# Optimization experiments

Measured on AMD Instinct MI355X. Metric: run time of the kernel, lower is better.

Reference implementation:

```python
import jax, jax.numpy as jnp
import numpy as np

MAX_TIMESTEPS = 100
EPS_VAR = 1e-8
EPS_DEN = 1e-8

def setup_inputs() -> dict:
    key = jax.random.key(0)
    k1, k2, k3, k4, k5 = jax.random.split(key, 5)
    b, c, h, w = 64, 3, 256, 256
    data = jax.random.normal(k1, (b, c, h, w), dtype=jnp.float32)
    noise = jax.random.normal(k2, (b, c, h, w), dtype=jnp.float32)
    times = jax.random.uniform(k3, (b,), dtype=jnp.float32)
    pred_mean = jax.random.normal(k4, (b, c, h, w), dtype=jnp.float32)
    pred_log_var = jax.random.normal(k5, (b, c, h, w), dtype=jnp.float32)
    return {"data": data, "noise": noise, "times": times,
            "pred_mean": pred_mean, "pred_log_var": pred_log_var}

def reference(data, noise, times, pred_mean, pred_log_var):
    b = data.shape[0]
    # times scaled as in forward: t * (1 - max_timesteps^-1)
    t = times * (1.0 - MAX_TIMESTEPS ** (-1))          # [b]
    t4 = t[:, None, None, None]                         # [b,1,1,1]
    tb = t[:, None]                                     # [b,1]

    # noised = noise.lerp(data, t) = noise + t*(data - noise)
    noised = noise + t4 * (data - noise)                # [b,c,h,w]

    d_flat = data.reshape(b, -1)                        # [j, d]
    n_flat = noised.reshape(b, -1)                      # [b, d]

    # dist[b,j] = sum_chw (noised_b - t_b * data_j)^2 / (2 * var_b)
    # expanded to avoid materializing [b,j,c,h,w]:
    var = (1.0 - tb) ** 2 + EPS_VAR                     # [b,1]
    n2 = jnp.sum(n_flat * n_flat, axis=-1, keepdims=True)   # [b,1]
    d2 = jnp.sum(d_flat * d_flat, axis=-1)                   # [j]
    cross = n_flat @ d_flat.T                                # [b,j]
    dist = (n2 - 2.0 * tb * cross + (tb ** 2) * d2[None, :]) / (2.0 * var)

    weights = jax.nn.softmax(-dist, axis=1)             # [b,j]

    # u_hat = sum_j w_bj (data_j - noised_b) / (1 - t_b + eps)
    #       = (weights @ data - noised) / (1 - t_b + eps)   (weights row-sum to 1)
    mix = weights @ d_flat                              # [b,d]
    u_hat = ((mix - n_flat) / (1.0 - tb + EPS_DEN)).reshape(data.shape)

    flow_cond = data - noise
    correction = jax.lax.stop_gradient(u_hat ** 2 - flow_cond ** 2)

    pred_var = jnp.exp(pred_log_var)
    loss = ((pred_mean - flow_cond) ** 2 / (2.0 * pred_var)
            + 0.5 * pred_log_var
            + correction / (2.0 * pred_var))
    loss = jax.lax.stop_gradient(pred_var) * loss
    return loss.mean()
```

## Files before the change

### kernel.cpp

```cpp
#include <hip/hip_runtime.h>
#include <cstdint>

namespace {

constexpr int BB = 64;
constexpr int DDIM = 196608;
constexpr float T_SCALE = 0.99f;

constexpr int WS_ZD   = 0;
constexpr int WS_DD   = 4096;
constexpr int WS_Z2   = 8192;
constexpr int WS_ELEM = 8256;
constexpr int NRED    = 8257;
constexpr int WS_U2   = 8320;
constexpr int WS_BIGP = 8384;
constexpr int PSTRIDE = 8272;

using f32x4  = __attribute__((ext_vector_type(4))) float;
using bf16x8 = __attribute__((ext_vector_type(8))) __bf16;

__device__ inline f32x4 MFMA(bf16x8 a, bf16x8 b, f32x4 c) {
  return __builtin_amdgcn_mfma_f32_16x16x32_bf16(a, b, c, 0, 0, 0);
}

__global__ void k_init(float* __restrict__ ws) {
  int idx = blockIdx.x * 256 + threadIdx.x;
  if (idx < NRED) ws[idx] = 0.0f;
}

template <int SUBT, bool ATOMIC>
__global__ __launch_bounds__(512) void k_main(
    const float* __restrict__ data, const float* __restrict__ noise,
    const float* __restrict__ pmean, const float* __restrict__ plogv,
    float* __restrict__ ws, float* __restrict__ bigp) {
  __shared__ __align__(16) short lds[6 * 4096];
  __shared__ float esm[8];

  const int t  = threadIdx.x;
  const int wv = t >> 6;
  const int l  = t & 63;
  const int g  = wv >> 2;
  const int m0 = (wv & 3) << 4;
  const int sr = t >> 3;
  const int c0 = t & 7;
  const int chunk0 = blockIdx.x * (SUBT << 6);
  float* dst = ATOMIC ? ws : (bigp + (size_t)blockIdx.x * PSTRIDE);

  f32x4 acc[4];
#pragma unroll
  for (int b = 0; b < 4; ++b) acc[b] = 0.0f;
  float z2acc = 0.0f, eacc = 0.0f;
  float4 dv[2], zv[2], pv[2], gv[2];
  uint4 sZ[3], sD[3];

  auto LOAD = [&](int s) {
    const size_t base = (size_t)sr * DDIM + chunk0 + (s << 6) + (c0 << 3);
#pragma unroll
    for (int i = 0; i < 2; ++i) {
      dv[i] = *(const float4*)(data  + base + (i << 2));
      zv[i] = *(const float4*)(noise + base + (i << 2));
      pv[i] = *(const float4*)(pmean + base + (i << 2));
      gv[i] = *(const float4*)(plogv + base + (i << 2));
    }
  };

  auto SPLIT8 = [&](const float4* v, uint4& H, uint4& M, uint4& L) {
    uint32_t h[4], m[4], lo[4];
    const float* f = (const float*)v;
#pragma unroll
    for (int p = 0; p < 4; ++p) {
      const float a = f[2 * p], b = f[2 * p + 1];
      const uint32_t ha = __float_as_uint(a) & 0xFFFF0000u;
      const uint32_t hb = __float_as_uint(b) & 0xFFFF0000u;
      h[p] = (ha >> 16) | hb;
      const float ra = a - __uint_as_float(ha);
      const float rb = b - __uint_as_float(hb);
      const uint32_t ma = __float_as_uint(ra) & 0xFFFF0000u;
      const uint32_t mb = __float_as_uint(rb) & 0xFFFF0000u;
      m[p] = (ma >> 16) | mb;
      const float sa = ra - __uint_as_float(ma);
      const float sb = rb - __uint_as_float(mb);
      lo[p] = (__float_as_uint(sa) >> 16) | (__float_as_uint(sb) & 0xFFFF0000u);
    }
    H = uint4{h[0], h[1], h[2], h[3]};
    M = uint4{m[0], m[1], m[2], m[3]};
    L = uint4{lo[0], lo[1], lo[2], lo[3]};
  };

  auto SPLITCALC = [&]() {
    const float* df = (const float*)dv;
    const float* zf = (const float*)zv;
    const float* pf = (const float*)pv;
    const float* gf = (const float*)gv;
#pragma unroll
    for (int p = 0; p < 8; ++p) {
      const float d = df[p], z = zf[p], pm = pf[p], pl = gf[p];
      const float fc = d - z;
      eacc += 0.5f * (pm * pm + __expf(pl) * pl) - pm * fc;
      z2acc += z * z;
    }
    SPLIT8(zv, sZ[0], sZ[1], sZ[2]);
    SPLIT8(dv, sD[0], sD[1], sD[2]);
  };

  auto DSW = [&]() {
    char* base = (char*)lds + sr * 128 + ((c0 ^ (sr & 7)) << 4);
#pragma unroll
    for (int sp = 0; sp < 3; ++sp) {
      *(uint4*)(base + sp * 8192)       = sZ[sp];
      *(uint4*)(base + (3 + sp) * 8192) = sD[sp];
    }
  };

  auto MMA = [&]() {
#pragma unroll
    for (int s2 = 0; s2 < 2; ++s2) {
      const int rA   = m0 + (l & 15);
      const int cA   = (s2 << 2) + (l >> 4);
      const int offA = rA * 128 + ((cA ^ (rA & 7)) << 4);
      bf16x8 af[3];
#pragma unroll
      for (int sp = 0; sp < 3; ++sp)
        af[sp] = *(const bf16x8*)((const char*)lds + (g * 3 + sp) * 8192 + offA);
#pragma unroll
      for (int b = 0; b < 4; ++b) {
        const int rB   = (b << 4) + (l & 15);
        const int offB = rB * 128 + ((cA ^ (rB & 7)) << 4);
        bf16x8 bd[3];
#pragma unroll
        for (int sp = 0; sp < 3; ++sp)
          bd[sp] = *(const bf16x8*)((const char*)lds + (3 + sp) * 8192 + offB);
        acc[b] = MFMA(af[0], bd[0], acc[b]);
        acc[b] = MFMA(af[0], bd[1], acc[b]);
        acc[b] = MFMA(af[1], bd[0], acc[b]);
        acc[b] = MFMA(af[1], bd[1], acc[b]);
        acc[b] = MFMA(af[0], bd[2], acc[b]);
        acc[b] = MFMA(af[2], bd[0], acc[b]);
      }
    }
  };

  LOAD(0);
  SPLITCALC();
  DSW();
  LOAD(1);
  __syncthreads();

  for (int s = 0; s < SUBT; ++s) {
    if (s + 1 < SUBT) SPLITCALC();
    MMA();
    __syncthreads();
    if (s + 1 < SUBT) {
      DSW();
      if (s + 2 < SUBT) LOAD(s + 2);
      __syncthreads();
    }
  }

  {
    float v = z2acc;
    v += __shfl_xor(v, 1);
    v += __shfl_xor(v, 2);
    v += __shfl_xor(v, 4);
    if ((l & 7) == 0) {
      if (ATOMIC) atomicAdd(ws + WS_Z2 + sr, v);
      else        dst[WS_Z2 + sr] = v;
    }
  }
  {
    float ev = eacc;
#pragma unroll
    for (int m = 1; m <= 32; m <<= 1) ev += __shfl_xor(ev, m);
    if (l == 0) esm[wv] = ev;
  }
  __syncthreads();
  if (t == 0) {
    float s0 = 0.f;
#pragma unroll
    for (int e = 0; e < 8; ++e) s0 += esm[e];
    if (ATOMIC) atomicAdd(ws + WS_ELEM, s0);
    else        dst[WS_ELEM] = s0;
  }

  const int grOff = (g == 0) ? WS_ZD : WS_DD;
#pragma unroll
  for (int b = 0; b < 4; ++b)
#pragma unroll
    for (int rg = 0; rg < 4; ++rg) {
      const int row = m0 + ((l >> 4) << 2) + rg;
      const int col = (b << 4) + (l & 15);
      if (ATOMIC) atomicAdd(ws + grOff + row * 64 + col, acc[b][rg]);
      else        dst[grOff + row * 64 + col] = acc[b][rg];
    }
}

__global__ void k_reduce(const float* __restrict__ bigp, float* __restrict__ ws,
                         int nb) {
  const int idx = blockIdx.x * 64 + threadIdx.x;
  if (idx >= NRED) return;
  const int per = nb >> 3;
  const size_t b0 = (size_t)blockIdx.y * per;
  float s = 0.f;
#pragma unroll 4
  for (int b = 0; b < per; ++b)
    s += bigp[(b0 + b) * PSTRIDE + idx];
  atomicAdd(ws + idx, s);
}

__global__ void k_small(const float* __restrict__ times, float* __restrict__ ws) {
  const int i = blockIdx.x;
  const int j = threadIdx.x;
  const double tt = (double)(times[i] * T_SCALE);
  const double omt = 1.0 - tt;
  const double var = omt * omt + 1e-8;
  const double inv2v = 1.0 / (2.0 * var);
  const double zd = (double)ws[WS_ZD + (i << 6) + j];
  const double dd = (double)ws[WS_DD + (i << 6) + j];
  const double cross = omt * zd + tt * dd;
  const double d2j = (double)ws[WS_DD + j * 65];
  const double lg = (2.0 * tt * cross - tt * tt * d2j) * inv2v;
  double m = lg;
#pragma unroll
  for (int msk = 1; msk <= 32; msk <<= 1) m = fmax(m, __shfl_xor(m, msk));
  const double e = exp(lg - m);
  double S = e;
#pragma unroll
  for (int msk = 1; msk <= 32; msk <<= 1) S += __shfl_xor(S, msk);
  const double wgt = e / S;

  __shared__ double wsh[64];
  wsh[j] = wgt;
  __syncthreads();
  double inner = 0.0;
#pragma unroll 8
  for (int j2 = 0; j2 < 64; ++j2)
    inner += wsh[j2] * (double)ws[WS_DD + (j << 6) + j2];
  double s1 = wgt * inner;
  double s2 = wgt * cross;
#pragma unroll
  for (int msk = 1; msk <= 32; msk <<= 1) {
    s1 += __shfl_xor(s1, msk);
    s2 += __shfl_xor(s2, msk);
  }
  if (j == 0) {
    const double zdii = (double)ws[WS_ZD + i * 65];
    const double d2i  = (double)ws[WS_DD + i * 65];
    const double z2i  = (double)ws[WS_Z2 + i];
    const double n2   = omt * omt * z2i + 2.0 * tt * omt * zdii + tt * tt * d2i;
    const double den  = omt + 1e-8;
    ws[WS_U2 + i] = (float)((s1 - 2.0 * s2 + n2) / (den * den));
  }
}

__global__ void k_final(const float* __restrict__ ws, float* __restrict__ out) {
  const int t = threadIdx.x;
  double v = 0.5 * (double)ws[WS_U2 + t];
  if (t == 0) v += (double)ws[WS_ELEM];
#pragma unroll
  for (int m = 1; m <= 32; m <<= 1) v += __shfl_xor(v, m);
  if (t == 0) out[0] = (float)(v / (double)((size_t)BB * DDIM));
}

}

extern "C" void kernel_launch(void* const* d_in, const int* in_sizes, int n_in,
                              void* d_out, int out_size, void* d_ws, size_t ws_size,
                              hipStream_t stream) {
  const float* data  = (const float*)d_in[0];
  const float* noise = (const float*)d_in[1];
  const float* times = (const float*)d_in[2];
  const float* pmean = (const float*)d_in[3];
  const float* plogv = (const float*)d_in[4];
  float* out = (float*)d_out;
  float* ws  = (float*)d_ws;
  float* bigp = ws + WS_BIGP;

  const bool fits512 =
      ws_size >= ((size_t)WS_BIGP + (size_t)512 * PSTRIDE) * sizeof(float);

  k_init<<<dim3(33), dim3(256), 0, stream>>>(ws);
  if (fits512) {
    k_main<6, false><<<dim3(512), dim3(512), 0, stream>>>(
        data, noise, pmean, plogv, ws, bigp);
    k_reduce<<<dim3(130, 8), dim3(64), 0, stream>>>(bigp, ws, 512);
  } else {
    k_main<6, true><<<dim3(512), dim3(512), 0, stream>>>(
        data, noise, pmean, plogv, ws, bigp);
  }
  k_small<<<dim3(64), dim3(64), 0, stream>>>(times, ws);
  k_final<<<dim3(1), dim3(64), 0, stream>>>(ws, out);
}
```

Baseline: 58.84 us.

## Double-buffer LDS with smaller K-steps and fuse softmax and final kernels

The main kernel now stages 32-column K-slices into two alternating LDS buffers, so each step needs one barrier instead of two. Global loads of the next slice overlap the MFMA work on the current one, and SUBT doubles so the per-block coverage stays the same. The small softmax kernel and the final reduction are merged into one 1024-thread launch that uses shuffles instead of shared memory for the weights, which removes one kernel launch. In exchange each thread does narrower 8-byte LDS writes, the MFMA batches per step are smaller, and the fused tail runs as a single block.

```diff
diff --git a/kernel.cpp b/kernel.cpp
--- a/kernel.cpp
+++ b/kernel.cpp
@@ -12,7 +12,6 @@
 constexpr int WS_Z2   = 8192;
 constexpr int WS_ELEM = 8256;
 constexpr int NRED    = 8257;
-constexpr int WS_U2   = 8320;
 constexpr int WS_BIGP = 8384;
 constexpr int PSTRIDE = 8272;
 
@@ -33,7 +32,7 @@
     const float* __restrict__ data, const float* __restrict__ noise,
     const float* __restrict__ pmean, const float* __restrict__ plogv,
     float* __restrict__ ws, float* __restrict__ bigp) {
-  __shared__ __align__(16) short lds[6 * 4096];
+  __shared__ __align__(16) char lds[49152];
   __shared__ float esm[8];
 
   const int t  = threadIdx.x;
@@ -41,34 +40,28 @@
   const int l  = t & 63;
   const int g  = wv >> 2;
   const int m0 = (wv & 3) << 4;
-  const int sr = t >> 3;
-  const int c0 = t & 7;
-  const int chunk0 = blockIdx.x * (SUBT << 6);
+  const int r  = t >> 3;
+  const int c4 = t & 7;
+  const int chunk0 = blockIdx.x * (SUBT * 32);
   float* dst = ATOMIC ? ws : (bigp + (size_t)blockIdx.x * PSTRIDE);
 
   f32x4 acc[4];
 #pragma unroll
   for (int b = 0; b < 4; ++b) acc[b] = 0.0f;
   float z2acc = 0.0f, eacc = 0.0f;
-  float4 dv[2], zv[2], pv[2], gv[2];
-  uint4 sZ[3], sD[3];
-
-  auto LOAD = [&](int s) {
-    const size_t base = (size_t)sr * DDIM + chunk0 + (s << 6) + (c0 << 3);
-#pragma unroll
-    for (int i = 0; i < 2; ++i) {
-      dv[i] = *(const float4*)(data  + base + (i << 2));
-      zv[i] = *(const float4*)(noise + base + (i << 2));
-      pv[i] = *(const float4*)(pmean + base + (i << 2));
-      gv[i] = *(const float4*)(plogv + base + (i << 2));
-    }
-  };
-
-  auto SPLIT8 = [&](const float4* v, uint4& H, uint4& M, uint4& L) {
-    uint32_t h[4], m[4], lo[4];
-    const float* f = (const float*)v;
-#pragma unroll
-    for (int p = 0; p < 4; ++p) {
+  float4 dv, zv;
+
+  auto LOADDZ = [&](int s) {
+    const size_t off = (size_t)r * DDIM + chunk0 + (s << 5) + (c4 << 2);
+    dv = *(const float4*)(data  + off);
+    zv = *(const float4*)(noise + off);
+  };
+
+  auto SPLITW = [&](int buf, const float4& v, int tbase) {
+    const float* f = (const float*)&v;
+    uint32_t h[2], m[2], lo[2];
+#pragma unroll
+    for (int p = 0; p < 2; ++p) {
       const float a = f[2 * p], b = f[2 * p + 1];
       const uint32_t ha = __float_as_uint(a) & 0xFFFF0000u;
       const uint32_t hb = __float_as_uint(b) & 0xFFFF0000u;
@@ -82,79 +75,75 @@
       const float sb = rb - __uint_as_float(mb);
       lo[p] = (__float_as_uint(sa) >> 16) | (__float_as_uint(sb) & 0xFFFF0000u);
     }
-    H = uint4{h[0], h[1], h[2], h[3]};
-    M = uint4{m[0], m[1], m[2], m[3]};
-    L = uint4{lo[0], lo[1], lo[2], lo[3]};
-  };
-
-  auto SPLITCALC = [&]() {
-    const float* df = (const float*)dv;
-    const float* zf = (const float*)zv;
-    const float* pf = (const float*)pv;
-    const float* gf = (const float*)gv;
-#pragma unroll
-    for (int p = 0; p < 8; ++p) {
+#pragma unroll
+    for (int sp = 0; sp < 3; ++sp) {
+      const int tile = tbase + sp;
+      const int byte = buf + ((tile >> 1) << 13) + (r << 7) +
+                       (((((tile & 1) << 2) + (c4 >> 1)) ^ (r & 7)) << 4) +
+                       ((c4 & 1) << 3);
+      const uint32_t* pk = (sp == 0) ? h : (sp == 1) ? m : lo;
+      *(uint2*)(lds + byte) = uint2{pk[0], pk[1]};
+    }
+  };
+
+  auto STAGE = [&](int s) {
+    const int buf = (s & 1) * 24576;
+    const size_t off = (size_t)r * DDIM + chunk0 + (s << 5) + (c4 << 2);
+    const float4 pm4 = *(const float4*)(pmean + off);
+    const float4 pl4 = *(const float4*)(plogv + off);
+    SPLITW(buf, zv, 0);
+    SPLITW(buf, dv, 3);
+    const float* df = (const float*)&dv;
+    const float* zf = (const float*)&zv;
+    const float* pf = (const float*)&pm4;
+    const float* gf = (const float*)&pl4;
+#pragma unroll
+    for (int p = 0; p < 4; ++p) {
       const float d = df[p], z = zf[p], pm = pf[p], pl = gf[p];
-      const float fc = d - z;
-      eacc += 0.5f * (pm * pm + __expf(pl) * pl) - pm * fc;
+      eacc += 0.5f * (pm * pm + __expf(pl) * pl) - pm * (d - z);
       z2acc += z * z;
     }
-    SPLIT8(zv, sZ[0], sZ[1], sZ[2]);
-    SPLIT8(dv, sD[0], sD[1], sD[2]);
-  };
-
-  auto DSW = [&]() {
-    char* base = (char*)lds + sr * 128 + ((c0 ^ (sr & 7)) << 4);
-#pragma unroll
-    for (int sp = 0; sp < 3; ++sp) {
-      *(uint4*)(base + sp * 8192)       = sZ[sp];
-      *(uint4*)(base + (3 + sp) * 8192) = sD[sp];
-    }
-  };
-
-  auto MMA = [&]() {
-#pragma unroll
-    for (int s2 = 0; s2 < 2; ++s2) {
-      const int rA   = m0 + (l & 15);
-      const int cA   = (s2 << 2) + (l >> 4);
-      const int offA = rA * 128 + ((cA ^ (rA & 7)) << 4);
-      bf16x8 af[3];
-#pragma unroll
-      for (int sp = 0; sp < 3; ++sp)
-        af[sp] = *(const bf16x8*)((const char*)lds + (g * 3 + sp) * 8192 + offA);
-#pragma unroll
-      for (int b = 0; b < 4; ++b) {
-        const int rB   = (b << 4) + (l & 15);
-        const int offB = rB * 128 + ((cA ^ (rB & 7)) << 4);
-        bf16x8 bd[3];
-#pragma unroll
-        for (int sp = 0; sp < 3; ++sp)
-          bd[sp] = *(const bf16x8*)((const char*)lds + (3 + sp) * 8192 + offB);
-        acc[b] = MFMA(af[0], bd[0], acc[b]);
-        acc[b] = MFMA(af[0], bd[1], acc[b]);
-        acc[b] = MFMA(af[1], bd[0], acc[b]);
-        acc[b] = MFMA(af[1], bd[1], acc[b]);
-        acc[b] = MFMA(af[0], bd[2], acc[b]);
-        acc[b] = MFMA(af[2], bd[0], acc[b]);
-      }
-    }
-  };
-
-  LOAD(0);
-  SPLITCALC();
-  DSW();
-  LOAD(1);
+  };
+
+  auto FRAG = [&](int buf, int tile, int row) -> bf16x8 {
+    const int byte = buf + ((tile >> 1) << 13) + (row << 7) +
+                     (((((tile & 1) << 2) + (l >> 4)) ^ (row & 7)) << 4);
+    return *(const bf16x8*)(lds + byte);
+  };
+
+  auto MMA = [&](int s) {
+    const int buf = (s & 1) * 24576;
+    const int ar  = m0 + (l & 15);
+    bf16x8 af[3];
+#pragma unroll
+    for (int sp = 0; sp < 3; ++sp) af[sp] = FRAG(buf, g * 3 + sp, ar);
+#pragma unroll
+    for (int b = 0; b < 4; ++b) {
+      const int br = (b << 4) + (l & 15);
+      bf16x8 bd[3];
+#pragma unroll
+      for (int sp = 0; sp < 3; ++sp) bd[sp] = FRAG(buf, 3 + sp, br);
+      acc[b] = MFMA(af[0], bd[0], acc[b]);
+      acc[b] = MFMA(af[0], bd[1], acc[b]);
+      acc[b] = MFMA(af[1], bd[0], acc[b]);
+      acc[b] = MFMA(af[1], bd[1], acc[b]);
+      acc[b] = MFMA(af[0], bd[2], acc[b]);
+      acc[b] = MFMA(af[2], bd[0], acc[b]);
+    }
+  };
+
+  LOADDZ(0);
+  STAGE(0);
+  LOADDZ(1);
   __syncthreads();
 
   for (int s = 0; s < SUBT; ++s) {
-    if (s + 1 < SUBT) SPLITCALC();
-    MMA();
+    if (s + 1 < SUBT) {
+      STAGE(s + 1);
+      if (s + 2 < SUBT) LOADDZ(s + 2);
+    }
+    MMA(s);
     __syncthreads();
-    if (s + 1 < SUBT) {
-      DSW();
-      if (s + 2 < SUBT) LOAD(s + 2);
-      __syncthreads();
-    }
   }
 
   {
@@ -163,8 +152,8 @@
     v += __shfl_xor(v, 2);
     v += __shfl_xor(v, 4);
     if ((l & 7) == 0) {
-      if (ATOMIC) atomicAdd(ws + WS_Z2 + sr, v);
-      else        dst[WS_Z2 + sr] = v;
+      if (ATOMIC) atomicAdd(ws + WS_Z2 + r, v);
+      else        dst[WS_Z2 + r] = v;
     }
   }
   {
@@ -207,58 +196,63 @@
   atomicAdd(ws + idx, s);
 }
 
-__global__ void k_small(const float* __restrict__ times, float* __restrict__ ws) {
-  const int i = blockIdx.x;
-  const int j = threadIdx.x;
-  const double tt = (double)(times[i] * T_SCALE);
-  const double omt = 1.0 - tt;
-  const double var = omt * omt + 1e-8;
-  const double inv2v = 1.0 / (2.0 * var);
-  const double zd = (double)ws[WS_ZD + (i << 6) + j];
-  const double dd = (double)ws[WS_DD + (i << 6) + j];
-  const double cross = omt * zd + tt * dd;
-  const double d2j = (double)ws[WS_DD + j * 65];
-  const double lg = (2.0 * tt * cross - tt * tt * d2j) * inv2v;
-  double m = lg;
-#pragma unroll
-  for (int msk = 1; msk <= 32; msk <<= 1) m = fmax(m, __shfl_xor(m, msk));
-  const double e = exp(lg - m);
-  double S = e;
-#pragma unroll
-  for (int msk = 1; msk <= 32; msk <<= 1) S += __shfl_xor(S, msk);
-  const double wgt = e / S;
-
-  __shared__ double wsh[64];
-  wsh[j] = wgt;
+__global__ __launch_bounds__(1024) void k_smallfinal(
+    const float* __restrict__ times, const float* __restrict__ ws,
+    float* __restrict__ out) {
+  __shared__ double u2s[64];
+  const int t = threadIdx.x;
+  const int wv = t >> 6;
+  const int j = t & 63;
+
+#pragma unroll
+  for (int ii = 0; ii < 4; ++ii) {
+    const int i = (wv << 2) + ii;
+    const double tt = (double)(times[i] * T_SCALE);
+    const double omt = 1.0 - tt;
+    const double var = omt * omt + 1e-8;
+    const double inv2v = 1.0 / (2.0 * var);
+    const double zd = (double)ws[WS_ZD + (i << 6) + j];
+    const double dd = (double)ws[WS_DD + (i << 6) + j];
+    const double cross = omt * zd + tt * dd;
+    const double d2j = (double)ws[WS_DD + j * 65];
+    const double lg = (2.0 * tt * cross - tt * tt * d2j) * inv2v;
+    double m = lg;
+#pragma unroll
+    for (int msk = 1; msk <= 32; msk <<= 1) m = fmax(m, __shfl_xor(m, msk));
+    const double e = exp(lg - m);
+    double S = e;
+#pragma unroll
+    for (int msk = 1; msk <= 32; msk <<= 1) S += __shfl_xor(S, msk);
+    const double wgt = e / S;
+
+    double inner = 0.0;
+#pragma unroll 8
+    for (int j2 = 0; j2 < 64; ++j2)
+      inner += __shfl(wgt, j2) * (double)ws[WS_DD + (j << 6) + j2];
+    double s1 = wgt * inner;
+    double s2 = wgt * cross;
+#pragma unroll
+    for (int msk = 1; msk <= 32; msk <<= 1) {
+      s1 += __shfl_xor(s1, msk);
+      s2 += __shfl_xor(s2, msk);
+    }
+    if (j == 0) {
+      const double zdii = (double)ws[WS_ZD + i * 65];
+      const double d2i  = (double)ws[WS_DD + i * 65];
+      const double z2i  = (double)ws[WS_Z2 + i];
+      const double n2 = omt * omt * z2i + 2.0 * tt * omt * zdii + tt * tt * d2i;
+      const double den = omt + 1e-8;
+      u2s[i] = (s1 - 2.0 * s2 + n2) / (den * den);
+    }
+  }
   __syncthreads();
-  double inner = 0.0;
-#pragma unroll 8
-  for (int j2 = 0; j2 < 64; ++j2)
-    inner += wsh[j2] * (double)ws[WS_DD + (j << 6) + j2];
-  double s1 = wgt * inner;
-  double s2 = wgt * cross;
-#pragma unroll
-  for (int msk = 1; msk <= 32; msk <<= 1) {
-    s1 += __shfl_xor(s1, msk);
-    s2 += __shfl_xor(s2, msk);
-  }
-  if (j == 0) {
-    const double zdii = (double)ws[WS_ZD + i * 65];
-    const double d2i  = (double)ws[WS_DD + i * 65];
-    const double z2i  = (double)ws[WS_Z2 + i];
-    const double n2   = omt * omt * z2i + 2.0 * tt * omt * zdii + tt * tt * d2i;
-    const double den  = omt + 1e-8;
-    ws[WS_U2 + i] = (float)((s1 - 2.0 * s2 + n2) / (den * den));
-  }
-}
-
-__global__ void k_final(const float* __restrict__ ws, float* __restrict__ out) {
-  const int t = threadIdx.x;
-  double v = 0.5 * (double)ws[WS_U2 + t];
-  if (t == 0) v += (double)ws[WS_ELEM];
-#pragma unroll
-  for (int m = 1; m <= 32; m <<= 1) v += __shfl_xor(v, m);
-  if (t == 0) out[0] = (float)(v / (double)((size_t)BB * DDIM));
+  if (wv == 0) {
+    double v = 0.5 * u2s[j];
+    if (j == 0) v += (double)ws[WS_ELEM];
+#pragma unroll
+    for (int m = 1; m <= 32; m <<= 1) v += __shfl_xor(v, m);
+    if (j == 0) out[0] = (float)(v / (double)((size_t)BB * DDIM));
+  }
 }
 
 }
@@ -280,13 +274,12 @@
 
   k_init<<<dim3(33), dim3(256), 0, stream>>>(ws);
   if (fits512) {
-    k_main<6, false><<<dim3(512), dim3(512), 0, stream>>>(
+    k_main<12, false><<<dim3(512), dim3(512), 0, stream>>>(
         data, noise, pmean, plogv, ws, bigp);
     k_reduce<<<dim3(130, 8), dim3(64), 0, stream>>>(bigp, ws, 512);
   } else {
-    k_main<6, true><<<dim3(512), dim3(512), 0, stream>>>(
+    k_main<12, true><<<dim3(512), dim3(512), 0, stream>>>(
         data, noise, pmean, plogv, ws, bigp);
   }
-  k_small<<<dim3(64), dim3(64), 0, stream>>>(times, ws);
-  k_final<<<dim3(1), dim3(64), 0, stream>>>(ws, out);
-}
+  k_smallfinal<<<dim3(1), dim3(1024), 0, stream>>>(times, ws, out);
+}
```

New measurement: 84.35 us. +43.4%, slower.

## Fuse small tail kernels, drop init launch, rebalance main grid to 768 blocks

Applied to the files above, without the earlier changes.

Merges the per-sample softmax kernel and the final reduction into one single-block kernel that uses shuffles instead of shared memory for the weights. The partial-sum reducer now writes its result directly with a block-level reduction instead of atomics, so the zero-init launch is no longer needed on the non-atomic path. The main kernel grid moves from 512 to 768 blocks with a smaller per-block subtile count. Together these cut two kernel launches and change load balance, at the cost of more partial rows to reduce and a serial 64-sample loop in a single block.

```diff
diff --git a/kernel.cpp b/kernel.cpp
--- a/kernel.cpp
+++ b/kernel.cpp
@@ -12,9 +12,9 @@
 constexpr int WS_Z2   = 8192;
 constexpr int WS_ELEM = 8256;
 constexpr int NRED    = 8257;
-constexpr int WS_U2   = 8320;
 constexpr int WS_BIGP = 8384;
 constexpr int PSTRIDE = 8272;
+constexpr int NB_MAIN = 768;
 
 using f32x4  = __attribute__((ext_vector_type(4))) float;
 using bf16x8 = __attribute__((ext_vector_type(8))) __bf16;
@@ -194,71 +194,82 @@
     }
 }
 
-__global__ void k_reduce(const float* __restrict__ bigp, float* __restrict__ ws,
-                         int nb) {
-  const int idx = blockIdx.x * 64 + threadIdx.x;
-  if (idx >= NRED) return;
-  const int per = nb >> 3;
-  const size_t b0 = (size_t)blockIdx.y * per;
+__global__ __launch_bounds__(256) void k_reduce(const float* __restrict__ bigp,
+                                                float* __restrict__ ws, int nb) {
+  __shared__ float red[4][64];
+  const int t = threadIdx.x;
+  const int wv = t >> 6, l = t & 63;
+  const int idx = blockIdx.x * 64 + l;
+  const int per = nb >> 2;
   float s = 0.f;
+  if (idx < NRED) {
+    const float* p = bigp + (size_t)wv * per * PSTRIDE + idx;
 #pragma unroll 4
-  for (int b = 0; b < per; ++b)
-    s += bigp[(b0 + b) * PSTRIDE + idx];
-  atomicAdd(ws + idx, s);
-}
-
-__global__ void k_small(const float* __restrict__ times, float* __restrict__ ws) {
-  const int i = blockIdx.x;
-  const int j = threadIdx.x;
-  const double tt = (double)(times[i] * T_SCALE);
-  const double omt = 1.0 - tt;
-  const double var = omt * omt + 1e-8;
-  const double inv2v = 1.0 / (2.0 * var);
-  const double zd = (double)ws[WS_ZD + (i << 6) + j];
-  const double dd = (double)ws[WS_DD + (i << 6) + j];
-  const double cross = omt * zd + tt * dd;
-  const double d2j = (double)ws[WS_DD + j * 65];
-  const double lg = (2.0 * tt * cross - tt * tt * d2j) * inv2v;
-  double m = lg;
-#pragma unroll
-  for (int msk = 1; msk <= 32; msk <<= 1) m = fmax(m, __shfl_xor(m, msk));
-  const double e = exp(lg - m);
-  double S = e;
-#pragma unroll
-  for (int msk = 1; msk <= 32; msk <<= 1) S += __shfl_xor(S, msk);
-  const double wgt = e / S;
-
-  __shared__ double wsh[64];
-  wsh[j] = wgt;
+    for (int b = 0; b < per; ++b) s += p[(size_t)b * PSTRIDE];
+  }
+  red[wv][l] = s;
   __syncthreads();
-  double inner = 0.0;
+  if (wv == 0 && idx < NRED)
+    ws[idx] = red[0][l] + red[1][l] + red[2][l] + red[3][l];
+}
+
+__global__ __launch_bounds__(1024) void k_smallfinal(
+    const float* __restrict__ times, const float* __restrict__ ws,
+    float* __restrict__ out) {
+  __shared__ double u2s[64];
+  const int t = threadIdx.x;
+  const int wv = t >> 6;
+  const int j = t & 63;
+
+#pragma unroll
+  for (int ii = 0; ii < 4; ++ii) {
+    const int i = (wv << 2) + ii;
+    const double tt = (double)(times[i] * T_SCALE);
+    const double omt = 1.0 - tt;
+    const double var = omt * omt + 1e-8;
+    const double inv2v = 1.0 / (2.0 * var);
+    const double zd = (double)ws[WS_ZD + (i << 6) + j];
+    const double dd = (double)ws[WS_DD + (i << 6) + j];
+    const double cross = omt * zd + tt * dd;
+    const double d2j = (double)ws[WS_DD + j * 65];
+    const double lg = (2.0 * tt * cross - tt * tt * d2j) * inv2v;
+    double m = lg;
+#pragma unroll
+    for (int msk = 1; msk <= 32; msk <<= 1) m = fmax(m, __shfl_xor(m, msk));
+    const double e = exp(lg - m);
+    double S = e;
+#pragma unroll
+    for (int msk = 1; msk <= 32; msk <<= 1) S += __shfl_xor(S, msk);
+    const double wgt = e / S;
+
+    double inner = 0.0;
 #pragma unroll 8
-  for (int j2 = 0; j2 < 64; ++j2)
-    inner += wsh[j2] * (double)ws[WS_DD + (j << 6) + j2];
-  double s1 = wgt * inner;
-  double s2 = wgt * cross;
-#pragma unroll
-  for (int msk = 1; msk <= 32; msk <<= 1) {
-    s1 += __shfl_xor(s1, msk);
-    s2 += __shfl_xor(s2, msk);
-  }
-  if (j == 0) {
-    const double zdii = (double)ws[WS_ZD + i * 65];
-    const double d2i  = (double)ws[WS_DD + i * 65];
-    const double z2i  = (double)ws[WS_Z2 + i];
-    const double n2   = omt * omt * z2i + 2.0 * tt * omt * zdii + tt * tt * d2i;
-    const double den  = omt + 1e-8;
-    ws[WS_U2 + i] = (float)((s1 - 2.0 * s2 + n2) / (den * den));
-  }
-}
-
-__global__ void k_final(const float* __restrict__ ws, float* __restrict__ out) {
-  const int t = threadIdx.x;
-  double v = 0.5 * (double)ws[WS_U2 + t];
-  if (t == 0) v += (double)ws[WS_ELEM];
-#pragma unroll
-  for (int m = 1; m <= 32; m <<= 1) v += __shfl_xor(v, m);
-  if (t == 0) out[0] = (float)(v / (double)((size_t)BB * DDIM));
+    for (int j2 = 0; j2 < 64; ++j2)
+      inner += __shfl(wgt, j2) * (double)ws[WS_DD + (j << 6) + j2];
+    double s1 = wgt * inner;
+    double s2 = wgt * cross;
+#pragma unroll
+    for (int msk = 1; msk <= 32; msk <<= 1) {
+      s1 += __shfl_xor(s1, msk);
+      s2 += __shfl_xor(s2, msk);
+    }
+    if (j == 0) {
+      const double zdii = (double)ws[WS_ZD + i * 65];
+      const double d2i  = (double)ws[WS_DD + i * 65];
+      const double z2i  = (double)ws[WS_Z2 + i];
+      const double n2 = omt * omt * z2i + 2.0 * tt * omt * zdii + tt * tt * d2i;
+      const double den = omt + 1e-8;
+      u2s[i] = (s1 - 2.0 * s2 + n2) / (den * den);
+    }
+  }
+  __syncthreads();
+  if (wv == 0) {
+    double v = 0.5 * u2s[j];
+    if (j == 0) v += (double)ws[WS_ELEM];
+#pragma unroll
+    for (int m = 1; m <= 32; m <<= 1) v += __shfl_xor(v, m);
+    if (j == 0) out[0] = (float)(v / (double)((size_t)BB * DDIM));
+  }
 }
 
 }
@@ -275,18 +286,17 @@
   float* ws  = (float*)d_ws;
   float* bigp = ws + WS_BIGP;
 
-  const bool fits512 =
-      ws_size >= ((size_t)WS_BIGP + (size_t)512 * PSTRIDE) * sizeof(float);
-
-  k_init<<<dim3(33), dim3(256), 0, stream>>>(ws);
-  if (fits512) {
-    k_main<6, false><<<dim3(512), dim3(512), 0, stream>>>(
+  const bool fits =
+      ws_size >= ((size_t)WS_BIGP + (size_t)NB_MAIN * PSTRIDE) * sizeof(float);
+
+  if (fits) {
+    k_main<4, false><<<dim3(NB_MAIN), dim3(512), 0, stream>>>(
         data, noise, pmean, plogv, ws, bigp);
-    k_reduce<<<dim3(130, 8), dim3(64), 0, stream>>>(bigp, ws, 512);
+    k_reduce<<<dim3(130), dim3(256), 0, stream>>>(bigp, ws, NB_MAIN);
   } else {
-    k_main<6, true><<<dim3(512), dim3(512), 0, stream>>>(
+    k_init<<<dim3(33), dim3(256), 0, stream>>>(ws);
+    k_main<4, true><<<dim3(NB_MAIN), dim3(512), 0, stream>>>(
         data, noise, pmean, plogv, ws, bigp);
   }
-  k_small<<<dim3(64), dim3(64), 0, stream>>>(times, ws);
-  k_final<<<dim3(1), dim3(64), 0, stream>>>(ws, out);
-}
+  k_smallfinal<<<dim3(1), dim3(1024), 0, stream>>>(times, ws, out);
+}
```

After: 93.70 us. 59.3% more time.
